# Optimization experiments

Hardware: AMD Instinct MI355X
Metric: run time of the kernel (lower is better)

## Reference

```python
import jax, jax.numpy as jnp
import numpy as np


def _conv3x3(x, w, b):
    # standard 3x3 conv, stride 1, padding 1, NCHW/OIHW
    y = jax.lax.conv_general_dilated(
        x, w, window_strides=(1, 1), padding=((1, 1), (1, 1)),
        dimension_numbers=('NCHW', 'OIHW', 'NCHW'))
    return y + b[None, :, None, None]


def _deform_conv3x3(x, offset, w, b):
    # torchvision-style DeformConv2d: kernel 3x3, stride 1, pad 1, dilation 1,
    # 1 offset group, no mask. offset: [B, 18, H, W] with (dy, dx) per tap.
    B, C, H, W = x.shape
    K = 9
    off = offset.reshape(B, K, 2, H, W)
    ky = (jnp.arange(K) // 3 - 1).astype(x.dtype)[None, :, None, None]
    kx = (jnp.arange(K) % 3 - 1).astype(x.dtype)[None, :, None, None]
    # fractional sample positions per output pixel and kernel tap: [B, K, H, W]
    sy = off[:, :, 0] + ky + jnp.arange(H, dtype=x.dtype)[None, None, :, None]
    sx = off[:, :, 1] + kx + jnp.arange(W, dtype=x.dtype)[None, None, None, :]
    y0f = jnp.floor(sy)
    x0f = jnp.floor(sx)
    dy = sy - y0f
    dx = sx - x0f
    y0 = y0f.astype(jnp.int32)
    x0 = x0f.astype(jnp.int32)

    def sample_b(xb, yi, xi):
        # xb: [C,H,W], yi/xi: [K,H,W] -> [C,K,H,W], zero outside bounds
        valid = (yi >= 0) & (yi < H) & (xi >= 0) & (xi < W)
        yc = jnp.clip(yi, 0, H - 1)
        xc = jnp.clip(xi, 0, W - 1)
        return xb[:, yc, xc] * valid[None].astype(xb.dtype)

    def bilinear_b(xb, y0b, x0b, dyb, dxb):
        v00 = sample_b(xb, y0b, x0b)
        v01 = sample_b(xb, y0b, x0b + 1)
        v10 = sample_b(xb, y0b + 1, x0b)
        v11 = sample_b(xb, y0b + 1, x0b + 1)
        w00 = ((1 - dyb) * (1 - dxb))[None]
        w01 = ((1 - dyb) * dxb)[None]
        w10 = (dyb * (1 - dxb))[None]
        w11 = (dyb * dxb)[None]
        return v00 * w00 + v01 * w01 + v10 * w10 + v11 * w11

    samp = jax.vmap(bilinear_b)(x, y0, x0, dy, dx)  # [B, C, K, H, W]
    Co, Ci = w.shape[0], w.shape[1]
    out = jnp.einsum('oik,bikhw->bohw', w.reshape(Co, Ci, K), samp)
    return out + b[None, :, None, None]


def setup_inputs() -> dict:
    key = jax.random.key(0)
    ks = jax.random.split(key, 5)
    B, C, H, W = 4, 128, 96, 96
    lr = jax.random.normal(ks[0], (B, C, H, W), jnp.float32)
    hr = jax.random.normal(ks[1], (B, C, H, W), jnp.float32)
    w_off = jax.random.normal(ks[2], (18, 2 * C, 3, 3), jnp.float32) * 0.02
    b_off = jnp.zeros((18,), jnp.float32)
    w_def = jax.random.normal(ks[3], (C, C, 3, 3), jnp.float32) / np.float32(np.sqrt(C * 9))
    b_def = jax.random.normal(ks[4], (C,), jnp.float32) * 0.01
    return {"lr_features": lr, "hr_features": hr, "w_off": w_off,
            "b_off": b_off, "w_def": w_def, "b_def": b_def}


def reference(lr_features, hr_features, w_off, b_off, w_def, b_def):
    inp = jnp.concatenate([lr_features, hr_features], axis=1)  # [B, 2C, H, W]
    offset = _conv3x3(inp, w_off, b_off)                        # [B, 18, H, W]
    return _deform_conv3x3(hr_features, offset, w_def, b_def)   # [B, C, H, W]
```

## Files before the change

kernel.cpp:

```cpp
#include <hip/hip_runtime.h>
#include <hip/hip_bf16.h>

#define HH 96
#define WW 96
#define CC 128
#define C2 256
#define PLANE (HH*WW)
#define NGRP 6
#define GP 8
#define NG 16
#define KSG 72
#define ROWS 13
#define NPCHK (ROWS*WW)
#define PCHK_PAD 1280

typedef __attribute__((ext_vector_type(8))) short bf16x8;
typedef __attribute__((ext_vector_type(4))) float f32x4;
typedef __attribute__((ext_vector_type(4))) unsigned int u32x4;

__device__ __forceinline__ int swz(int row, int byte_in_row) {
    return row * 128 + (byte_in_row ^ ((row & 7) << 4));
}

__device__ __forceinline__ void gload_lds16(const void* g, void* l) {
    __builtin_amdgcn_global_load_lds(
        (const __attribute__((address_space(1))) char*)g,
        (__attribute__((address_space(3))) char*)l, 16, 0, 0);
}

__device__ __forceinline__ unsigned pack2(float a, float b) {
    return (unsigned)__bfloat16_as_ushort(__float2bfloat16(a)) |
           ((unsigned)__bfloat16_as_ushort(__float2bfloat16(b)) << 16);
}

#define MFMA16(A,B,C) __builtin_amdgcn_mfma_f32_16x16x32_bf16((A),(B),(C),0,0,0)

#define VMW4() { asm volatile("s_waitcnt vmcnt(4)" ::: "memory"); __builtin_amdgcn_sched_barrier(0); }
#define VMW0() { asm volatile("s_waitcnt vmcnt(0)" ::: "memory"); __builtin_amdgcn_sched_barrier(0); }
#define LGKM0_BAR() { asm volatile("s_waitcnt lgkmcnt(0)" ::: "memory"); \
    __builtin_amdgcn_sched_barrier(0); __builtin_amdgcn_s_barrier(); \
    __builtin_amdgcn_sched_barrier(0); }
#define RAW_BAR() { __builtin_amdgcn_sched_barrier(0); __builtin_amdgcn_s_barrier(); \
    __builtin_amdgcn_sched_barrier(0); }

__global__ __launch_bounds__(256) void prep_kernel(
    const float* __restrict__ hr, const float* __restrict__ lr,
    const float* __restrict__ w_def, const float* __restrict__ w_off,
    unsigned short* __restrict__ hrbf, unsigned short* __restrict__ lrbf,
    unsigned short* __restrict__ wpad, unsigned short* __restrict__ wop)
{
    const int bid = blockIdx.x;
    const int tid = threadIdx.x;
    if (bid < 4608) {
        const bool is_hr = bid < 2304;
        const float* src0 = is_hr ? hr : lr;
        unsigned short* o = is_hr ? hrbf : lrbf;
        int idx = (is_hr ? bid : bid - 2304) * 256 + tid;
        int hw = idx % PLANE;
        int t  = idx / PLANE;
        int g  = t & 15;
        int b  = t >> 4;
        const float* src = src0 + ((size_t)(b * CC + g * GP)) * PLANE + hw;
        unsigned pk[4];
#pragma unroll
        for (int j = 0; j < 4; ++j)
            pk[j] = pack2(src[(size_t)(2*j) * PLANE], src[(size_t)(2*j+1) * PLANE]);
        u32x4 v = {pk[0], pk[1], pk[2], pk[3]};
        *reinterpret_cast<u32x4*>(o + (size_t)idx * 8) = v;
    } else if (bid < 5184) {
        int i = (bid - 4608) * 256 + tid;
        int oc = i / (NG * KSG);
        int r  = i - oc * (NG * KSG);
        int g  = r / KSG;
        int s  = r - g * KSG;
        int tap = s >> 3;
        int icoff = s & 7;
        wpad[i] = __bfloat16_as_ushort(__float2bfloat16(
            w_def[(size_t)(oc * CC + g * GP + icoff) * 9 + tap]));
    } else {
        int i = (bid - 5184) * 256 + tid;
        int oc = i / (32 * KSG);
        int r  = i - oc * (32 * KSG);
        int g  = r / KSG;
        int s  = r - g * KSG;
        int tap = s >> 3;
        int icoff = s & 7;
        int c = g * 8 + icoff;
        float v = (oc < 18) ? w_off[(size_t)(oc * C2 + c) * 9 + tap] : 0.f;
        wop[i] = __bfloat16_as_ushort(__float2bfloat16(v));
    }
}

__global__ __launch_bounds__(256) void wcvt_kernel(const float* __restrict__ w,
                                                   unsigned short* __restrict__ o)
{
    int i = blockIdx.x * 256 + threadIdx.x;
    if (i < CC * NG * KSG) {
        int oc = i / (NG * KSG);
        int r  = i - oc * (NG * KSG);
        int g  = r / KSG;
        int s  = r - g * KSG;
        int tap = s >> 3;
        int icoff = s & 7;
        o[i] = __bfloat16_as_ushort(__float2bfloat16(
            w[(size_t)(oc * CC + g * GP + icoff) * 9 + tap]));
    }
}

__global__ __launch_bounds__(256) void cvt8_kernel(const float* __restrict__ src0,
                                                   unsigned short* __restrict__ o)
{
    int idx = blockIdx.x * 256 + threadIdx.x;
    int hw = idx % PLANE;
    int t  = idx / PLANE;
    int g  = t & 15;
    int b  = t >> 4;
    const float* src = src0 + ((size_t)(b * CC + g * GP)) * PLANE + hw;
    unsigned pk[4];
#pragma unroll
    for (int j = 0; j < 4; ++j)
        pk[j] = pack2(src[(size_t)(2*j) * PLANE], src[(size_t)(2*j+1) * PLANE]);
    u32x4 v = {pk[0], pk[1], pk[2], pk[3]};
    *reinterpret_cast<u32x4*>(o + (size_t)idx * 8) = v;
}

__global__ __launch_bounds__(256) void offset_conv_kernel(
    const float* __restrict__ lr, const float* __restrict__ hr,
    const float* __restrict__ w_off, float* __restrict__ outp)
{
    __shared__ float tile[2][324];
    const int bid = blockIdx.x;
    const int q   = bid % NGRP;
    const int t   = bid / NGRP;
    const int b   = t / 36;
    const int rr  = t % 36;
    const int h0  = (rr / 6) * 16;
    const int w0  = (rr % 6) * 16;
    const int tid = threadIdx.x;
    const int py  = tid >> 4;
    const int px  = tid & 15;

    const int c0 = (C2 * q) / NGRP, c1 = (C2 * (q + 1)) / NGRP;
    const float* srcp = (q < 3) ? lr : hr;
    const int cofs = (q < 3) ? 0 : CC;

    int gy0 = h0 - 1 + tid / 18, gx0 = w0 - 1 + tid % 18;
    bool ok0 = (unsigned)gy0 < (unsigned)HH && (unsigned)gx0 < (unsigned)WW;
    int off0 = gy0 * WW + gx0;
    int j1 = tid + 256;
    int gy1 = h0 - 1 + j1 / 18, gx1 = w0 - 1 + j1 % 18;
    bool ok1 = (j1 < 324) && (unsigned)gy1 < (unsigned)HH && (unsigned)gx1 < (unsigned)WW;
    int off1 = gy1 * WW + gx1;

    float acc[18];
#pragma unroll
    for (int oc = 0; oc < 18; ++oc) acc[oc] = 0.f;

    const float* pl = srcp + (size_t)(b * CC + c0 - cofs) * PLANE;
    float p0 = ok0 ? pl[off0] : 0.f;
    float p1 = ok1 ? pl[off1] : 0.f;

    for (int c = c0; c < c1; ++c) {
        float* tb = tile[c & 1];
        tb[tid] = p0;
        if (j1 < 324) tb[j1] = p1;
        __syncthreads();
        if (c + 1 < c1) {
            const float* pn = srcp + (size_t)(b * CC + c + 1 - cofs) * PLANE;
            p0 = ok0 ? pn[off0] : 0.f;
            p1 = ok1 ? pn[off1] : 0.f;
        }
        float tv[9];
#pragma unroll
        for (int ky = 0; ky < 3; ++ky)
#pragma unroll
            for (int kx = 0; kx < 3; ++kx)
                tv[ky*3+kx] = tb[(py+ky)*18 + px + kx];
#pragma unroll
        for (int oc = 0; oc < 18; ++oc) {
            const float* wp = w_off + (size_t)(oc * C2 + c) * 9;
#pragma unroll
            for (int tap = 0; tap < 9; ++tap)
                acc[oc] = fmaf(wp[tap], tv[tap], acc[oc]);
        }
    }
#pragma unroll
    for (int oc = 0; oc < 18; ++oc)
        outp[((size_t)(b*CC + q*18 + oc)) * PLANE + (h0+py)*WW + (w0+px)] = acc[oc];
}

__global__ __launch_bounds__(768, 6) void offset_mfma_kernel(
    const unsigned short* __restrict__ lrbf, const unsigned short* __restrict__ hrbf,
    const unsigned short* __restrict__ wop, const float* __restrict__ b_off,
    float* __restrict__ offw)
{
    __shared__ __align__(16) unsigned short planes[2][2][3*WW*8];
    __shared__ __align__(16) unsigned short wgt0[2][32*64];
    __shared__ __align__(16) unsigned short wgt1[2][32*8];
    __shared__ __align__(16) unsigned short samp0[2][WW*64];
    __shared__ __align__(16) unsigned short samp1[2][WW*8];

    const int rawb = blockIdx.x;
    const int bid  = (rawb & 7) * 48 + (rawb >> 3);
    const int b    = bid / HH;
    const int h    = bid % HH;
    const int tid  = threadIdx.x;

    const int pri = tid / 96, ppx = tid - (tid / 96) * 96;
    const int prow = min(max(h - 1 + pri, 0), HH - 1);

    const int woc = tid / 9, wsl = tid % 9;
    float4 wv0, wv1;

#define ISSUE_P2(PAIR, PB) { \
    if (tid < 288) { \
        int gA_ = 2*(PAIR), gB_ = gA_ + 1; \
        const unsigned short* bA_ = (gA_ < 16 ? lrbf : hrbf); \
        const unsigned short* bB_ = (gB_ < 16 ? lrbf : hrbf); \
        gload_lds16(bA_ + ((size_t)(b*16 + (gA_ & 15)) * PLANE + prow*WW + ppx) * 8, \
                    (char*)planes[PB][0] + tid*16); \
        gload_lds16(bB_ + ((size_t)(b*16 + (gB_ & 15)) * PLANE + prow*WW + ppx) * 8, \
                    (char*)planes[PB][1] + tid*16); \
    } }
#define ISSUE_W2(PAIR) { \
    if (tid < 288) { \
        wv0 = *reinterpret_cast<const float4*>(wop + ((size_t)(woc*32 + 2*(PAIR)    ))*KSG + wsl*8); \
        wv1 = *reinterpret_cast<const float4*>(wop + ((size_t)(woc*32 + 2*(PAIR) + 1))*KSG + wsl*8); \
    } }
#define WRITE_W2() { \
    if (tid < 288) { \
        if (wsl < 8) { \
            *reinterpret_cast<float4*>((char*)wgt0[0] + swz(woc, wsl*16)) = wv0; \
            *reinterpret_cast<float4*>((char*)wgt0[1] + swz(woc, wsl*16)) = wv1; \
        } else { \
            *reinterpret_cast<float4*>((char*)wgt1[0] + woc*16) = wv0; \
            *reinterpret_cast<float4*>((char*)wgt1[1] + woc*16) = wv1; \
        } \
    } }

    const int tap1 = tid / WW, px1 = tid - (tid / WW) * WW;
    const int ky1 = tap1 / 3 - 1, kx1 = tap1 % 3 - 1;
    const int row1 = h + ky1, x1 = px1 + kx1;
    const bool ok1 = (unsigned)row1 < (unsigned)HH && (unsigned)x1 < (unsigned)WW;
    const int ro1 = ((ky1+1)*WW + x1) * 16;
    const int wr1 = px1*128 + ((tap1*16) ^ ((px1 & 7) << 4));
    const int x2 = tid + 1;
    const bool ok2 = (tid < 96) && (h + 1 < HH) && (x2 < WW);
    const int ro2 = (2*WW + x2) * 16;
    const int wr2 = tid * 16;

    const int lane = tid & 63;
    const int wid  = tid >> 6;
    const int ocg  = wid / 6;
    const int pxg  = wid - ocg * 6;
    const int l15  = lane & 15;
    const int l4   = lane >> 4;
    const int rowA = ocg*16 + l15;
    const int rowB = pxg*16 + l15;
    const bf16x8 zf = {};

    f32x4 acc = (f32x4){0.f, 0.f, 0.f, 0.f};

#define MFMA_O2() { \
    _Pragma("unroll") \
    for (int q_ = 0; q_ < 2; ++q_) { \
        bf16x8 a0_ = *reinterpret_cast<const bf16x8*>((char*)wgt0[q_] + swz(rowA, l4*16)); \
        bf16x8 a1_ = *reinterpret_cast<const bf16x8*>((char*)wgt0[q_] + swz(rowA, 64 + l4*16)); \
        bf16x8 a2_ = *reinterpret_cast<const bf16x8*>((char*)wgt1[q_] + rowA*16); \
        if (l4) a2_ = zf; \
        bf16x8 b0_ = *reinterpret_cast<const bf16x8*>((char*)samp0[q_] + swz(rowB, l4*16)); \
        bf16x8 b1_ = *reinterpret_cast<const bf16x8*>((char*)samp0[q_] + swz(rowB, 64 + l4*16)); \
        bf16x8 b2_ = *reinterpret_cast<const bf16x8*>((char*)samp1[q_] + rowB*16); \
        acc = MFMA16(a0_, b0_, acc); \
        acc = MFMA16(a1_, b1_, acc); \
        acc = MFMA16(a2_, b2_, acc); \
    } }

    ISSUE_W2(0);
    ISSUE_P2(0, 0);
    __syncthreads();

    for (int p2 = 0; p2 < 16; ++p2) {
        const int sb = p2 & 1;
        WRITE_W2();
        if (p2 < 15) {
            ISSUE_W2(p2 + 1);
            ISSUE_P2(p2 + 1, sb ^ 1);
            VMW4();
        } else {
            VMW0();
        }
        RAW_BAR();
        {
            u32x4 vA = {0u, 0u, 0u, 0u}, vB = {0u, 0u, 0u, 0u};
            if (ok1) {
                vA = *reinterpret_cast<const u32x4*>((const char*)planes[sb][0] + ro1);
                vB = *reinterpret_cast<const u32x4*>((const char*)planes[sb][1] + ro1);
            }
            *reinterpret_cast<u32x4*>((char*)samp0[0] + wr1) = vA;
            *reinterpret_cast<u32x4*>((char*)samp0[1] + wr1) = vB;
            if (tid < 96) {
                u32x4 wA = {0u, 0u, 0u, 0u}, wB = {0u, 0u, 0u, 0u};
                if (ok2) {
                    wA = *reinterpret_cast<const u32x4*>((const char*)planes[sb][0] + ro2);
                    wB = *reinterpret_cast<const u32x4*>((const char*)planes[sb][1] + ro2);
                }
                *reinterpret_cast<u32x4*>((char*)samp1[0] + wr2) = wA;
                *reinterpret_cast<u32x4*>((char*)samp1[1] + wr2) = wB;
            }
        }
        LGKM0_BAR();
        __builtin_amdgcn_s_setprio(1);
        MFMA_O2();
        __builtin_amdgcn_s_setprio(0);
        RAW_BAR();
    }

#pragma unroll
    for (int r = 0; r < 4; ++r) {
        int oc = ocg*16 + l4*4 + r;
        if (oc < 18)
            offw[((size_t)(b*18 + oc)) * PLANE + h*WW + pxg*16 + l15] = acc[r] + b_off[oc];
    }
#undef ISSUE_P2
#undef ISSUE_W2
#undef WRITE_W2
#undef MFMA_O2
}

__global__ __launch_bounds__(768, 6) void deform3_kernel(
    const unsigned short* __restrict__ hrbf, const unsigned short* __restrict__ wpad,
    const float* __restrict__ b_def, const float* __restrict__ offw,
    float* __restrict__ outp)
{
    __shared__ __align__(16) unsigned short wgt0[CC*64];
    __shared__ __align__(16) unsigned short wgt1[CC*8];
    __shared__ __align__(16) unsigned short samp0[WW*64];
    __shared__ __align__(16) unsigned short samp1[WW*8];
    __shared__ __align__(16) float4 gw4[9*WW];
    __shared__ __align__(8)  short4 gyo[9*WW];
    __shared__ float bias_lds[CC];

    const int rawb = blockIdx.x;
    const int bid  = (rawb & 7) * 48 + (rawb >> 3);
    const int b    = bid / HH;
    const int h    = bid % HH;
    const int tid  = threadIdx.x;

    float4 wv0, wv1;
    const int wc0oc = tid / 9, wc0s = tid % 9;
    const int wt2   = (tid < 384) ? tid + 768 : tid;
    const int wc1oc = wt2 / 9, wc1s = wt2 % 9;

#define ISSUE_WGT(G) { \
    wv0 = *reinterpret_cast<const float4*>(wpad + ((size_t)(wc0oc*NG + (G))*KSG + wc0s*8)); \
    wv1 = *reinterpret_cast<const float4*>(wpad + ((size_t)(wc1oc*NG + (G))*KSG + wc1s*8)); }
#define WRITE_WGT() { \
    if (wc0s < 8) *reinterpret_cast<float4*>((char*)wgt0 + swz(wc0oc, wc0s*16)) = wv0; \
    else          *reinterpret_cast<float4*>((char*)wgt1 + wc0oc*16) = wv0; \
    if (tid < 384) { \
        if (wc1s < 8) *reinterpret_cast<float4*>((char*)wgt0 + swz(wc1oc, wc1s*16)) = wv1; \
        else          *reinterpret_cast<float4*>((char*)wgt1 + wc1oc*16) = wv1; \
    } }

    ISSUE_WGT(0);

    for (int it = tid; it < 9 * WW; it += 768) {
        int tap = it / WW;
        int px  = it - tap * WW;
        int hw  = h * WW + px;
        float offy = offw[((size_t)(b*18 + 2*tap    )) * PLANE + hw];
        float offx = offw[((size_t)(b*18 + 2*tap + 1)) * PLANE + hw];
        float sy = (float)h  + (float)(tap/3 - 1) + offy;
        float sx = (float)px + (float)(tap%3 - 1) + offx;
        float y0f = floorf(sy), x0f = floorf(sx);
        float dy = sy - y0f, dx = sx - x0f;
        int y0 = (int)y0f, x0 = (int)x0f;
        bool y0v = (unsigned)y0       < (unsigned)HH;
        bool y1v = (unsigned)(y0 + 1) < (unsigned)HH;
        bool x0v = (unsigned)x0       < (unsigned)WW;
        bool x1v = (unsigned)(x0 + 1) < (unsigned)WW;
        float ody = 1.f - dy, odx = 1.f - dx;
        float4 wv;
        wv.x = (y0v && x0v) ? ody*odx : 0.f;
        wv.y = (y0v && x1v) ? ody*dx  : 0.f;
        wv.z = (y1v && x0v) ? dy*odx  : 0.f;
        wv.w = (y1v && x1v) ? dy*dx   : 0.f;
        short4 o4;
        o4.x = (short)min(max(y0,     0), HH-1);
        o4.y = (short)min(max(y0 + 1, 0), HH-1);
        o4.z = (short)min(max(x0,     0), WW-1);
        o4.w = (short)min(max(x0 + 1, 0), WW-1);
        gw4[it] = wv;
        gyo[it] = o4;
    }
    if (tid < CC) bias_lds[tid] = b_def[tid];
    __syncthreads();

    const int lane = tid & 63;
    const int wid  = tid >> 6;
    const int ocg4 = wid / 3;
    const int pxg  = wid - ocg4 * 3;
    const int l15  = lane & 15;
    const int l4   = lane >> 4;

    f32x4 acc[2][2];
#pragma unroll
    for (int mf = 0; mf < 2; ++mf)
#pragma unroll
        for (int nf = 0; nf < 2; ++nf)
            acc[mf][nf] = (f32x4){0.f, 0.f, 0.f, 0.f};

    const int rowA0 = ocg4*32 + l15, rowA1 = rowA0 + 16;
    const int rowB0 = pxg*32 + l15,  rowB1 = rowB0 + 16;
    const bf16x8 zf = {};

#define MFMA_G() { \
    bf16x8 a00_ = *reinterpret_cast<const bf16x8*>((char*)wgt0 + swz(rowA0, l4*16)); \
    bf16x8 a10_ = *reinterpret_cast<const bf16x8*>((char*)wgt0 + swz(rowA1, l4*16)); \
    bf16x8 a01_ = *reinterpret_cast<const bf16x8*>((char*)wgt0 + swz(rowA0, 64 + l4*16)); \
    bf16x8 a11_ = *reinterpret_cast<const bf16x8*>((char*)wgt0 + swz(rowA1, 64 + l4*16)); \
    bf16x8 a02_ = *reinterpret_cast<const bf16x8*>((char*)wgt1 + rowA0*16); \
    bf16x8 a12_ = *reinterpret_cast<const bf16x8*>((char*)wgt1 + rowA1*16); \
    if (l4) { a02_ = zf; a12_ = zf; } \
    const char* s0_ = (const char*)samp0; \
    const char* s1_ = (const char*)samp1; \
    bf16x8 b00_ = *reinterpret_cast<const bf16x8*>(s0_ + swz(rowB0, l4*16)); \
    bf16x8 b10_ = *reinterpret_cast<const bf16x8*>(s0_ + swz(rowB1, l4*16)); \
    bf16x8 b01_ = *reinterpret_cast<const bf16x8*>(s0_ + swz(rowB0, 64 + l4*16)); \
    bf16x8 b11_ = *reinterpret_cast<const bf16x8*>(s0_ + swz(rowB1, 64 + l4*16)); \
    bf16x8 b02_ = *reinterpret_cast<const bf16x8*>(s1_ + rowB0*16); \
    bf16x8 b12_ = *reinterpret_cast<const bf16x8*>(s1_ + rowB1*16); \
    acc[0][0] = MFMA16(a00_, b00_, acc[0][0]); \
    acc[0][1] = MFMA16(a00_, b10_, acc[0][1]); \
    acc[1][0] = MFMA16(a10_, b00_, acc[1][0]); \
    acc[1][1] = MFMA16(a10_, b10_, acc[1][1]); \
    acc[0][0] = MFMA16(a01_, b01_, acc[0][0]); \
    acc[0][1] = MFMA16(a01_, b11_, acc[0][1]); \
    acc[1][0] = MFMA16(a11_, b01_, acc[1][0]); \
    acc[1][1] = MFMA16(a11_, b11_, acc[1][1]); \
    acc[0][0] = MFMA16(a02_, b02_, acc[0][0]); \
    acc[0][1] = MFMA16(a02_, b12_, acc[0][1]); \
    acc[1][0] = MFMA16(a12_, b02_, acc[1][0]); \
    acc[1][1] = MFMA16(a12_, b12_, acc[1][1]); }

    const unsigned short* gb = hrbf + (size_t)(b * NG) * PLANE * 8;

    for (int g = 0; g < NG; ++g) {
        WRITE_WGT();
        if (g < NG - 1) ISSUE_WGT(g + 1);
        const unsigned short* gpl = gb + (size_t)g * PLANE * 8;
        for (int it = tid; it < 9 * WW; it += 768) {
            float4 w4 = gw4[it];
            short4 o4 = gyo[it];
            int ra = (int)o4.x * WW, rb = (int)o4.y * WW;
            u32x4 q00 = *reinterpret_cast<const u32x4*>(gpl + (size_t)(ra + o4.z) * 8);
            u32x4 q01 = *reinterpret_cast<const u32x4*>(gpl + (size_t)(ra + o4.w) * 8);
            u32x4 q10 = *reinterpret_cast<const u32x4*>(gpl + (size_t)(rb + o4.z) * 8);
            u32x4 q11 = *reinterpret_cast<const u32x4*>(gpl + (size_t)(rb + o4.w) * 8);
            float sv[GP];
#pragma unroll
            for (int j = 0; j < 4; ++j) {
                float a00 = __uint_as_float(q00[j] << 16), b00 = __uint_as_float(q00[j] & 0xffff0000u);
                float a01 = __uint_as_float(q01[j] << 16), b01 = __uint_as_float(q01[j] & 0xffff0000u);
                float a10 = __uint_as_float(q10[j] << 16), b10 = __uint_as_float(q10[j] & 0xffff0000u);
                float a11 = __uint_as_float(q11[j] << 16), b11 = __uint_as_float(q11[j] & 0xffff0000u);
                sv[2*j]   = fmaf(w4.x, a00, fmaf(w4.y, a01, fmaf(w4.z, a10, w4.w*a11)));
                sv[2*j+1] = fmaf(w4.x, b00, fmaf(w4.y, b01, fmaf(w4.z, b10, w4.w*b11)));
            }
            unsigned pk0 = pack2(sv[0], sv[1]), pk1 = pack2(sv[2], sv[3]);
            unsigned pk2 = pack2(sv[4], sv[5]), pk3 = pack2(sv[6], sv[7]);
            u32x4 pv = {pk0, pk1, pk2, pk3};
            int tap = it / WW;
            int px  = it - tap * WW;
            if (tap < 8)
                *reinterpret_cast<u32x4*>((char*)samp0 + swz(px, tap*16)) = pv;
            else
                *reinterpret_cast<u32x4*>((char*)samp1 + px*16) = pv;
        }
        LGKM0_BAR();
        __builtin_amdgcn_s_setprio(1);
        MFMA_G();
        __builtin_amdgcn_s_setprio(0);
        RAW_BAR();
    }

#pragma unroll
    for (int mf = 0; mf < 2; ++mf)
#pragma unroll
        for (int r = 0; r < 4; ++r) {
            int oc = ocg4*32 + mf*16 + l4*4 + r;
            float bd = bias_lds[oc];
#pragma unroll
            for (int nf = 0; nf < 2; ++nf) {
                int px = pxg*32 + nf*16 + l15;
                outp[((size_t)(b*CC + oc)) * PLANE + h*WW + px] = acc[mf][nf][r] + bd;
            }
        }
#undef ISSUE_WGT
#undef WRITE_WGT
#undef MFMA_G
}

template<bool HRBF, bool OFFWS>
__global__ __launch_bounds__(768, 6) void deform2_kernel(
    const float* __restrict__ hr, const unsigned short* __restrict__ hrbf,
    const float* __restrict__ b_off, const unsigned short* __restrict__ wpad,
    const float* __restrict__ b_def, const float* __restrict__ offw,
    float* __restrict__ outp)
{
    __shared__ __align__(16) unsigned short planes[2][PCHK_PAD*8];
    __shared__ __align__(16) unsigned short wgt0[CC*64];
    __shared__ __align__(16) unsigned short wgt1[CC*8];
    __shared__ __align__(16) unsigned short samp0[WW*64];
    __shared__ __align__(16) unsigned short samp1[WW*8];
    __shared__ __align__(8)  float2 geom[9*97];
    __shared__ float bias_lds[CC];

    const int rawb = blockIdx.x;
    const int bid  = (rawb & 7) * 48 + (rawb >> 3);
    const int b    = bid / HH;
    const int h    = bid % HH;
    const int tid  = threadIdx.x;
    const int r0   = min(max(h - 6, 0), HH - ROWS);

    const float* hrb = hr + (size_t)b * CC * PLANE;

    float4 wv0, wv1;
    const int wc0oc = tid / 9, wc0s = tid % 9;
    const int wt2   = (tid < 384) ? tid + 768 : tid;
    const int wc1oc = wt2 / 9, wc1s = wt2 % 9;
    const int pc2   = (tid < 512) ? tid + 768 : tid;
    const int pcs   = min(pc2, NPCHK - 1);

#define ISSUE_WGT(G) { \
    wv0 = *reinterpret_cast<const float4*>(wpad + ((size_t)(wc0oc*NG + (G))*KSG + wc0s*8)); \
    wv1 = *reinterpret_cast<const float4*>(wpad + ((size_t)(wc1oc*NG + (G))*KSG + wc1s*8)); }
#define WRITE_WGT() { \
    if (wc0s < 8) *reinterpret_cast<float4*>((char*)wgt0 + swz(wc0oc, wc0s*16)) = wv0; \
    else          *reinterpret_cast<float4*>((char*)wgt1 + wc0oc*16) = wv0; \
    if (tid < 384) { \
        if (wc1s < 8) *reinterpret_cast<float4*>((char*)wgt0 + swz(wc1oc, wc1s*16)) = wv1; \
        else          *reinterpret_cast<float4*>((char*)wgt1 + wc1oc*16) = wv1; \
    } }

#define ISSUE_PLANES(G, PB) { \
    const unsigned short* src_ = hrbf + ((size_t)(b*NG + (G))*PLANE + r0*WW)*8; \
    gload_lds16(src_ + (size_t)tid*8, (char*)planes[PB] + tid*16); \
    gload_lds16(src_ + (size_t)pcs*8, (char*)planes[PB] + pc2*16); }

#define STAGE_DIRECT(G, PB) { \
    for (int p = tid; p < NPCHK; p += 768) { \
        int r_ = p / WW, x_ = p - (p / WW) * WW; \
        const float* s_ = hrb + (size_t)((G)*GP) * PLANE + (r0 + r_)*WW + x_; \
        unsigned pk_[4]; \
        _Pragma("unroll") \
        for (int j = 0; j < 4; ++j) \
            pk_[j] = pack2(s_[(size_t)(2*j)*PLANE], s_[(size_t)(2*j+1)*PLANE]); \
        u32x4 v_ = {pk_[0], pk_[1], pk_[2], pk_[3]}; \
        *reinterpret_cast<u32x4*>((char*)planes[PB] + p*16) = v_; \
    } }

    if (HRBF) ISSUE_PLANES(0, 0);
    ISSUE_WGT(0);

    for (int t = tid; t < 9 * WW; t += 768) {
        int tap = t / WW;
        int px  = t - tap * WW;
        int hw  = h * WW + px;
        float offy, offx;
        if (OFFWS) {
            offy = offw[((size_t)(b*18 + 2*tap    )) * PLANE + hw];
            offx = offw[((size_t)(b*18 + 2*tap + 1)) * PLANE + hw];
        } else {
            offy = b_off[2*tap]; offx = b_off[2*tap + 1];
#pragma unroll
            for (int q = 0; q < NGRP; ++q) {
                offy += outp[((size_t)(b*CC + q*18 + 2*tap    )) * PLANE + hw];
                offx += outp[((size_t)(b*CC + q*18 + 2*tap + 1)) * PLANE + hw];
            }
        }
        geom[tap*97 + px] = make_float2((float)h  + (float)(tap/3 - 1) + offy,
                                        (float)px + (float)(tap%3 - 1) + offx);
    }
    if (tid < CC) bias_lds[tid] = b_def[tid];
    if (!HRBF) STAGE_DIRECT(0, 0);
    __syncthreads();

    const int lane = tid & 63;
    const int wid  = tid >> 6;
    const int ocg4 = wid / 3;
    const int pxg  = wid - ocg4 * 3;
    const int l15  = lane & 15;
    const int l4   = lane >> 4;

    f32x4 acc[2][2];
#pragma unroll
    for (int mf = 0; mf < 2; ++mf)
#pragma unroll
        for (int nf = 0; nf < 2; ++nf)
            acc[mf][nf] = (f32x4){0.f, 0.f, 0.f, 0.f};

    const int rowA0 = ocg4*32 + l15, rowA1 = rowA0 + 16;
    const int rowB0 = pxg*32 + l15,  rowB1 = rowB0 + 16;
    const bf16x8 zf = {};

#define MFMA_G() { \
    bf16x8 a00_ = *reinterpret_cast<const bf16x8*>((char*)wgt0 + swz(rowA0, l4*16)); \
    bf16x8 a10_ = *reinterpret_cast<const bf16x8*>((char*)wgt0 + swz(rowA1, l4*16)); \
    bf16x8 a01_ = *reinterpret_cast<const bf16x8*>((char*)wgt0 + swz(rowA0, 64 + l4*16)); \
    bf16x8 a11_ = *reinterpret_cast<const bf16x8*>((char*)wgt0 + swz(rowA1, 64 + l4*16)); \
    bf16x8 a02_ = *reinterpret_cast<const bf16x8*>((char*)wgt1 + rowA0*16); \
    bf16x8 a12_ = *reinterpret_cast<const bf16x8*>((char*)wgt1 + rowA1*16); \
    if (l4) { a02_ = zf; a12_ = zf; } \
    const char* s0_ = (const char*)samp0; \
    const char* s1_ = (const char*)samp1; \
    bf16x8 b00_ = *reinterpret_cast<const bf16x8*>(s0_ + swz(rowB0, l4*16)); \
    bf16x8 b10_ = *reinterpret_cast<const bf16x8*>(s0_ + swz(rowB1, l4*16)); \
    bf16x8 b01_ = *reinterpret_cast<const bf16x8*>(s0_ + swz(rowB0, 64 + l4*16)); \
    bf16x8 b11_ = *reinterpret_cast<const bf16x8*>(s0_ + swz(rowB1, 64 + l4*16)); \
    bf16x8 b02_ = *reinterpret_cast<const bf16x8*>(s1_ + rowB0*16); \
    bf16x8 b12_ = *reinterpret_cast<const bf16x8*>(s1_ + rowB1*16); \
    acc[0][0] = MFMA16(a00_, b00_, acc[0][0]); \
    acc[0][1] = MFMA16(a00_, b10_, acc[0][1]); \
    acc[1][0] = MFMA16(a10_, b00_, acc[1][0]); \
    acc[1][1] = MFMA16(a10_, b10_, acc[1][1]); \
    acc[0][0] = MFMA16(a01_, b01_, acc[0][0]); \
    acc[0][1] = MFMA16(a01_, b11_, acc[0][1]); \
    acc[1][0] = MFMA16(a11_, b01_, acc[1][0]); \
    acc[1][1] = MFMA16(a11_, b11_, acc[1][1]); \
    acc[0][0] = MFMA16(a02_, b02_, acc[0][0]); \
    acc[0][1] = MFMA16(a02_, b12_, acc[0][1]); \
    acc[1][0] = MFMA16(a12_, b02_, acc[1][0]); \
    acc[1][1] = MFMA16(a12_, b12_, acc[1][1]); }

    for (int g = 0; g < NG; ++g) {
        const int pb = g & 1;
        WRITE_WGT();
        if (g < NG - 1) {
            ISSUE_WGT(g + 1);
            if (HRBF) { ISSUE_PLANES(g + 1, pb ^ 1); }
            else      { STAGE_DIRECT(g + 1, pb ^ 1); }
            if (HRBF) { VMW4(); }
        } else {
            if (HRBF) { VMW0(); }
        }
        for (int it = tid; it < 9 * WW; it += 768) {
            int tap = it / WW;
            int px  = it - tap * WW;
            float2 s2 = geom[tap*97 + px];
            float sy = s2.x, sx = s2.y;
            float y0f = floorf(sy), x0f = floorf(sx);
            float dy = sy - y0f, dx = sx - x0f;
            int y0 = (int)y0f, x0 = (int)x0f;
            bool y0v = (unsigned)y0       < (unsigned)HH;
            bool y1v = (unsigned)(y0 + 1) < (unsigned)HH;
            bool x0v = (unsigned)x0       < (unsigned)WW;
            bool x1v = (unsigned)(x0 + 1) < (unsigned)WW;
            float ody = 1.f - dy, odx = 1.f - dx;
            float w00 = (y0v && x0v) ? ody*odx : 0.f;
            float w01 = (y0v && x1v) ? ody*dx  : 0.f;
            float w10 = (y1v && x0v) ? dy*odx  : 0.f;
            float w11 = (y1v && x1v) ? dy*dx   : 0.f;
            int y0c = min(max(y0, 0), HH-1), y1c = min(max(y0+1, 0), HH-1);
            int x0c = min(max(x0, 0), WW-1), x1c = min(max(x0+1, 0), WW-1);
            float sv[GP];
            bool ng = (y0v && (unsigned)(y0 - r0) >= (unsigned)ROWS) ||
                      (y1v && (unsigned)(y1c - r0) >= (unsigned)ROWS);
            if (__builtin_expect(!ng, 1)) {
                int ra = min(max(y0c - r0, 0), ROWS-1);
                int rb = min(max(y1c - r0, 0), ROWS-1);
                const char* pbase = (const char*)planes[pb];
                u32x4 q00 = *reinterpret_cast<const u32x4*>(pbase + (ra*WW + x0c)*16);
                u32x4 q01 = *reinterpret_cast<const u32x4*>(pbase + (ra*WW + x1c)*16);
                u32x4 q10 = *reinterpret_cast<const u32x4*>(pbase + (rb*WW + x0c)*16);
                u32x4 q11 = *reinterpret_cast<const u32x4*>(pbase + (rb*WW + x1c)*16);
#pragma unroll
                for (int j = 0; j < 4; ++j) {
                    float a00 = __uint_as_float(q00[j] << 16), b00 = __uint_as_float(q00[j] & 0xffff0000u);
                    float a01 = __uint_as_float(q01[j] << 16), b01 = __uint_as_float(q01[j] & 0xffff0000u);
                    float a10 = __uint_as_float(q10[j] << 16), b10 = __uint_as_float(q10[j] & 0xffff0000u);
                    float a11 = __uint_as_float(q11[j] << 16), b11 = __uint_as_float(q11[j] & 0xffff0000u);
                    sv[2*j]   = fmaf(w00, a00, fmaf(w01, a01, fmaf(w10, a10, w11*a11)));
                    sv[2*j+1] = fmaf(w00, b00, fmaf(w01, b01, fmaf(w10, b10, w11*b11)));
                }
            } else {
                const float* base = hrb + (size_t)(g*GP) * PLANE;
#pragma unroll
                for (int j = 0; j < GP; ++j) {
                    const float* p = base + (size_t)j * PLANE;
                    sv[j] = fmaf(w00, p[y0c*WW + x0c], fmaf(w01, p[y0c*WW + x1c],
                            fmaf(w10, p[y1c*WW + x0c], w11 * p[y1c*WW + x1c])));
                }
            }
            unsigned pk0 = pack2(sv[0], sv[1]), pk1 = pack2(sv[2], sv[3]);
            unsigned pk2 = pack2(sv[4], sv[5]), pk3 = pack2(sv[6], sv[7]);
            u32x4 pv = {pk0, pk1, pk2, pk3};
            if (tap < 8)
                *reinterpret_cast<u32x4*>((char*)samp0 + swz(px, tap*16)) = pv;
            else
                *reinterpret_cast<u32x4*>((char*)samp1 + px*16) = pv;
        }
        LGKM0_BAR();
        __builtin_amdgcn_s_setprio(1);
        MFMA_G();
        __builtin_amdgcn_s_setprio(0);
        RAW_BAR();
    }

#pragma unroll
    for (int mf = 0; mf < 2; ++mf)
#pragma unroll
        for (int r = 0; r < 4; ++r) {
            int oc = ocg4*32 + mf*16 + l4*4 + r;
            float bd = bias_lds[oc];
#pragma unroll
            for (int nf = 0; nf < 2; ++nf) {
                int px = pxg*32 + nf*16 + l15;
                outp[((size_t)(b*CC + oc)) * PLANE + h*WW + px] = acc[mf][nf][r] + bd;
            }
        }
#undef ISSUE_WGT
#undef WRITE_WGT
#undef ISSUE_PLANES
#undef STAGE_DIRECT
#undef MFMA_G
}

extern "C" void kernel_launch(void* const* d_in, const int* in_sizes, int n_in,
                              void* d_out, int out_size, void* d_ws, size_t ws_size,
                              hipStream_t stream)
{
    const float* lr    = (const float*)d_in[0];
    const float* hr    = (const float*)d_in[1];
    const float* w_off = (const float*)d_in[2];
    const float* b_off = (const float*)d_in[3];
    const float* w_def = (const float*)d_in[4];
    const float* b_def = (const float*)d_in[5];
    float* outp = (float*)d_out;

    const size_t wpad_b = (size_t)CC * NG * KSG * 2 + 256;
    const size_t hrbf_b = (size_t)4 * NG * PLANE * GP * 2;
    const size_t lrbf_b = hrbf_b;
    const size_t woff_b = (size_t)32 * 32 * KSG * 2 + 256;
    const size_t offw_b = (size_t)4 * 18 * PLANE * 4;

    unsigned short* wpad = (unsigned short*)d_ws;
    unsigned short* hrbf = (unsigned short*)((char*)d_ws + wpad_b);
    unsigned short* lrbf = (unsigned short*)((char*)d_ws + wpad_b + hrbf_b);
    unsigned short* wop  = (unsigned short*)((char*)d_ws + wpad_b + hrbf_b + lrbf_b);
    float*          offw = (float*)((char*)d_ws + wpad_b + hrbf_b + lrbf_b + woff_b);

    const bool full     = ws_size >= wpad_b + hrbf_b + lrbf_b + woff_b + offw_b;
    const bool use_hrbf = ws_size >= wpad_b + hrbf_b + lrbf_b;

    if (full) {
        prep_kernel<<<5472, 256, 0, stream>>>(hr, lr, w_def, w_off,
                                              hrbf, lrbf, wpad, wop);
        offset_mfma_kernel<<<4*HH, 768, 0, stream>>>(lrbf, hrbf, wop, b_off, offw);
        deform3_kernel<<<4*HH, 768, 0, stream>>>(hrbf, wpad, b_def, offw, outp);
    } else {
        wcvt_kernel<<<(CC*NG*KSG + 255)/256, 256, 0, stream>>>(w_def, wpad);
        if (use_hrbf)
            cvt8_kernel<<<(4*NG*PLANE)/256, 256, 0, stream>>>(hr, hrbf);
        offset_conv_kernel<<<4*36*NGRP, 256, 0, stream>>>(lr, hr, w_off, outp);
        if (use_hrbf)
            deform2_kernel<true, false><<<4*HH, 768, 0, stream>>>(
                hr, hrbf, b_off, wpad, b_def, offw, outp);
        else
            deform2_kernel<false, false><<<4*HH, 768, 0, stream>>>(
                hr, hrbf, b_off, wpad, b_def, offw, outp);
    }
}
```

Baseline: 91.54 us.

## Split deform kernel into half-row blocks of 384 threads with 64x16 warp tiles

Each deform block now covers half an output row (48 pixels) with 384 threads, and twice as many blocks are launched (768 instead of 384). Each wave computes 64 output channels by 16 pixels, reusing one B fragment across four A fragments. The aim is better CU fill, since 384 big blocks underfill the GPU, and finer-grained scheduling. In exchange, every block reloads the full weight slice per group, doubling total weight traffic and LDS weight writes.

Result: faster. 84.83 us, median of 2 (-7.3%).

```diff
diff --git a/kernel.cpp b/kernel.cpp
--- a/kernel.cpp
+++ b/kernel.cpp
@@ -13,6 +13,7 @@
 #define ROWS 13
 #define NPCHK (ROWS*WW)
 #define PCHK_PAD 1280
+#define HPX 48
 
 typedef __attribute__((ext_vector_type(8))) short bf16x8;
 typedef __attribute__((ext_vector_type(4))) float f32x4;
@@ -328,51 +329,56 @@
 #undef MFMA_O2
 }
 
-__global__ __launch_bounds__(768, 6) void deform3_kernel(
+__global__ __launch_bounds__(384, 6) void deform3_kernel(
     const unsigned short* __restrict__ hrbf, const unsigned short* __restrict__ wpad,
     const float* __restrict__ b_def, const float* __restrict__ offw,
     float* __restrict__ outp)
 {
     __shared__ __align__(16) unsigned short wgt0[CC*64];
     __shared__ __align__(16) unsigned short wgt1[CC*8];
-    __shared__ __align__(16) unsigned short samp0[WW*64];
-    __shared__ __align__(16) unsigned short samp1[WW*8];
-    __shared__ __align__(16) float4 gw4[9*WW];
-    __shared__ __align__(8)  short4 gyo[9*WW];
+    __shared__ __align__(16) unsigned short samp0[HPX*64];
+    __shared__ __align__(16) unsigned short samp1[HPX*8];
+    __shared__ __align__(16) float4 gw4[9*HPX];
+    __shared__ __align__(8)  short4 gyo[9*HPX];
     __shared__ float bias_lds[CC];
 
     const int rawb = blockIdx.x;
-    const int bid  = (rawb & 7) * 48 + (rawb >> 3);
-    const int b    = bid / HH;
-    const int h    = bid % HH;
+    const int bid  = (rawb & 7) * 96 + (rawb >> 3);
+    const int b    = bid / 192;
+    const int t2   = bid % 192;
+    const int h    = t2 >> 1;
+    const int half = t2 & 1;
+    const int px0  = half * HPX;
     const int tid  = threadIdx.x;
 
-    float4 wv0, wv1;
-    const int wc0oc = tid / 9, wc0s = tid % 9;
-    const int wt2   = (tid < 384) ? tid + 768 : tid;
-    const int wc1oc = wt2 / 9, wc1s = wt2 % 9;
+    float4 wv0, wv1, wv2;
+    const int c0 = tid,        w0oc = c0 / 9, w0s = c0 % 9;
+    const int c1 = tid + 384,  w1oc = c1 / 9, w1s = c1 % 9;
+    const int c2 = tid + 768,  w2oc = c2 / 9, w2s = c2 % 9;
 
 #define ISSUE_WGT(G) { \
-    wv0 = *reinterpret_cast<const float4*>(wpad + ((size_t)(wc0oc*NG + (G))*KSG + wc0s*8)); \
-    wv1 = *reinterpret_cast<const float4*>(wpad + ((size_t)(wc1oc*NG + (G))*KSG + wc1s*8)); }
+    wv0 = *reinterpret_cast<const float4*>(wpad + ((size_t)(w0oc*NG + (G))*KSG + w0s*8)); \
+    wv1 = *reinterpret_cast<const float4*>(wpad + ((size_t)(w1oc*NG + (G))*KSG + w1s*8)); \
+    wv2 = *reinterpret_cast<const float4*>(wpad + ((size_t)(w2oc*NG + (G))*KSG + w2s*8)); }
 #define WRITE_WGT() { \
-    if (wc0s < 8) *reinterpret_cast<float4*>((char*)wgt0 + swz(wc0oc, wc0s*16)) = wv0; \
-    else          *reinterpret_cast<float4*>((char*)wgt1 + wc0oc*16) = wv0; \
-    if (tid < 384) { \
-        if (wc1s < 8) *reinterpret_cast<float4*>((char*)wgt0 + swz(wc1oc, wc1s*16)) = wv1; \
-        else          *reinterpret_cast<float4*>((char*)wgt1 + wc1oc*16) = wv1; \
-    } }
+    if (w0s < 8) *reinterpret_cast<float4*>((char*)wgt0 + swz(w0oc, w0s*16)) = wv0; \
+    else         *reinterpret_cast<float4*>((char*)wgt1 + w0oc*16) = wv0; \
+    if (w1s < 8) *reinterpret_cast<float4*>((char*)wgt0 + swz(w1oc, w1s*16)) = wv1; \
+    else         *reinterpret_cast<float4*>((char*)wgt1 + w1oc*16) = wv1; \
+    if (w2s < 8) *reinterpret_cast<float4*>((char*)wgt0 + swz(w2oc, w2s*16)) = wv2; \
+    else         *reinterpret_cast<float4*>((char*)wgt1 + w2oc*16) = wv2; }
 
     ISSUE_WGT(0);
 
-    for (int it = tid; it < 9 * WW; it += 768) {
-        int tap = it / WW;
-        int px  = it - tap * WW;
-        int hw  = h * WW + px;
+    for (int it = tid; it < 9 * HPX; it += 384) {
+        int tap = it / HPX;
+        int px  = it - tap * HPX;
+        int gx  = px0 + px;
+        int hw  = h * WW + gx;
         float offy = offw[((size_t)(b*18 + 2*tap    )) * PLANE + hw];
         float offx = offw[((size_t)(b*18 + 2*tap + 1)) * PLANE + hw];
         float sy = (float)h  + (float)(tap/3 - 1) + offy;
-        float sx = (float)px + (float)(tap%3 - 1) + offx;
+        float sx = (float)gx + (float)(tap%3 - 1) + offx;
         float y0f = floorf(sy), x0f = floorf(sx);
         float dy = sy - y0f, dx = sx - x0f;
         int y0 = (int)y0f, x0 = (int)x0f;
@@ -399,50 +405,38 @@
 
     const int lane = tid & 63;
     const int wid  = tid >> 6;
-    const int ocg4 = wid / 3;
-    const int pxg  = wid - ocg4 * 3;
+    const int ocg  = wid / 3;
+    const int pxg  = wid - ocg * 3;
     const int l15  = lane & 15;
     const int l4   = lane >> 4;
 
-    f32x4 acc[2][2];
-#pragma unroll
-    for (int mf = 0; mf < 2; ++mf)
-#pragma unroll
-        for (int nf = 0; nf < 2; ++nf)
-            acc[mf][nf] = (f32x4){0.f, 0.f, 0.f, 0.f};
-
-    const int rowA0 = ocg4*32 + l15, rowA1 = rowA0 + 16;
-    const int rowB0 = pxg*32 + l15,  rowB1 = rowB0 + 16;
+    f32x4 acc[4];
+#pragma unroll
+    for (int mf = 0; mf < 4; ++mf) acc[mf] = (f32x4){0.f, 0.f, 0.f, 0.f};
+
+    const int rowB = pxg*16 + l15;
     const bf16x8 zf = {};
 
 #define MFMA_G() { \
-    bf16x8 a00_ = *reinterpret_cast<const bf16x8*>((char*)wgt0 + swz(rowA0, l4*16)); \
-    bf16x8 a10_ = *reinterpret_cast<const bf16x8*>((char*)wgt0 + swz(rowA1, l4*16)); \
-    bf16x8 a01_ = *reinterpret_cast<const bf16x8*>((char*)wgt0 + swz(rowA0, 64 + l4*16)); \
-    bf16x8 a11_ = *reinterpret_cast<const bf16x8*>((char*)wgt0 + swz(rowA1, 64 + l4*16)); \
-    bf16x8 a02_ = *reinterpret_cast<const bf16x8*>((char*)wgt1 + rowA0*16); \
-    bf16x8 a12_ = *reinterpret_cast<const bf16x8*>((char*)wgt1 + rowA1*16); \
-    if (l4) { a02_ = zf; a12_ = zf; } \
-    const char* s0_ = (const char*)samp0; \
-    const char* s1_ = (const char*)samp1; \
-    bf16x8 b00_ = *reinterpret_cast<const bf16x8*>(s0_ + swz(rowB0, l4*16)); \
-    bf16x8 b10_ = *reinterpret_cast<const bf16x8*>(s0_ + swz(rowB1, l4*16)); \
-    bf16x8 b01_ = *reinterpret_cast<const bf16x8*>(s0_ + swz(rowB0, 64 + l4*16)); \
-    bf16x8 b11_ = *reinterpret_cast<const bf16x8*>(s0_ + swz(rowB1, 64 + l4*16)); \
-    bf16x8 b02_ = *reinterpret_cast<const bf16x8*>(s1_ + rowB0*16); \
-    bf16x8 b12_ = *reinterpret_cast<const bf16x8*>(s1_ + rowB1*16); \
-    acc[0][0] = MFMA16(a00_, b00_, acc[0][0]); \
-    acc[0][1] = MFMA16(a00_, b10_, acc[0][1]); \
-    acc[1][0] = MFMA16(a10_, b00_, acc[1][0]); \
-    acc[1][1] = MFMA16(a10_, b10_, acc[1][1]); \
-    acc[0][0] = MFMA16(a01_, b01_, acc[0][0]); \
-    acc[0][1] = MFMA16(a01_, b11_, acc[0][1]); \
-    acc[1][0] = MFMA16(a11_, b01_, acc[1][0]); \
-    acc[1][1] = MFMA16(a11_, b11_, acc[1][1]); \
-    acc[0][0] = MFMA16(a02_, b02_, acc[0][0]); \
-    acc[0][1] = MFMA16(a02_, b12_, acc[0][1]); \
-    acc[1][0] = MFMA16(a12_, b02_, acc[1][0]); \
-    acc[1][1] = MFMA16(a12_, b12_, acc[1][1]); }
+    _Pragma("unroll") \
+    for (int ks = 0; ks < 2; ++ks) { \
+        int kb = ks*64 + l4*16; \
+        bf16x8 bb = *reinterpret_cast<const bf16x8*>((char*)samp0 + swz(rowB, kb)); \
+        _Pragma("unroll") \
+        for (int mf = 0; mf < 4; ++mf) { \
+            bf16x8 aa = *reinterpret_cast<const bf16x8*>((char*)wgt0 + swz(ocg*64 + mf*16 + l15, kb)); \
+            acc[mf] = MFMA16(aa, bb, acc[mf]); \
+        } \
+    } \
+    { \
+        bf16x8 bb = *reinterpret_cast<const bf16x8*>((char*)samp1 + rowB*16); \
+        _Pragma("unroll") \
+        for (int mf = 0; mf < 4; ++mf) { \
+            bf16x8 aa = *reinterpret_cast<const bf16x8*>((char*)wgt1 + (ocg*64 + mf*16 + l15)*16); \
+            if (l4) aa = zf; \
+            acc[mf] = MFMA16(aa, bb, acc[mf]); \
+        } \
+    } }
 
     const unsigned short* gb = hrbf + (size_t)(b * NG) * PLANE * 8;
 
@@ -450,7 +444,7 @@
         WRITE_WGT();
         if (g < NG - 1) ISSUE_WGT(g + 1);
         const unsigned short* gpl = gb + (size_t)g * PLANE * 8;
-        for (int it = tid; it < 9 * WW; it += 768) {
+        for (int it = tid; it < 9 * HPX; it += 384) {
             float4 w4 = gw4[it];
             short4 o4 = gyo[it];
             int ra = (int)o4.x * WW, rb = (int)o4.y * WW;
@@ -471,8 +465,8 @@
             unsigned pk0 = pack2(sv[0], sv[1]), pk1 = pack2(sv[2], sv[3]);
             unsigned pk2 = pack2(sv[4], sv[5]), pk3 = pack2(sv[6], sv[7]);
             u32x4 pv = {pk0, pk1, pk2, pk3};
-            int tap = it / WW;
-            int px  = it - tap * WW;
+            int tap = it / HPX;
+            int px  = it - tap * HPX;
             if (tap < 8)
                 *reinterpret_cast<u32x4*>((char*)samp0 + swz(px, tap*16)) = pv;
             else
@@ -486,16 +480,12 @@
     }
 
 #pragma unroll
-    for (int mf = 0; mf < 2; ++mf)
+    for (int mf = 0; mf < 4; ++mf)
 #pragma unroll
         for (int r = 0; r < 4; ++r) {
-            int oc = ocg4*32 + mf*16 + l4*4 + r;
+            int oc = ocg*64 + mf*16 + l4*4 + r;
             float bd = bias_lds[oc];
-#pragma unroll
-            for (int nf = 0; nf < 2; ++nf) {
-                int px = pxg*32 + nf*16 + l15;
-                outp[((size_t)(b*CC + oc)) * PLANE + h*WW + px] = acc[mf][nf][r] + bd;
-            }
+            outp[((size_t)(b*CC + oc)) * PLANE + h*WW + px0 + pxg*16 + l15] = acc[mf][r] + bd;
         }
 #undef ISSUE_WGT
 #undef WRITE_WGT
@@ -758,7 +748,7 @@
         prep_kernel<<<5472, 256, 0, stream>>>(hr, lr, w_def, w_off,
                                               hrbf, lrbf, wpad, wop);
         offset_mfma_kernel<<<4*HH, 768, 0, stream>>>(lrbf, hrbf, wop, b_off, offw);
-        deform3_kernel<<<4*HH, 768, 0, stream>>>(hrbf, wpad, b_def, offw, outp);
+        deform3_kernel<<<4*HH*2, 384, 0, stream>>>(hrbf, wpad, b_def, offw, outp);
     } else {
         wcvt_kernel<<<(CC*NG*KSG + 255)/256, 256, 0, stream>>>(w_def, wpad);
         if (use_hrbf)
```
